# Kernel tuning notes

Measured on AMD Instinct MI355X. Metric: run time of the kernel, lower is better.

## Reference

```python
import jax, jax.numpy as jnp
import numpy as np

INPUT_SIZE = 1024
MEMORY_SIZE = 32768
MEMORY_DIM = 128
TOP_K = 32
EPS = 1e-8


def _linear_params(key, fan_in, fan_out):
    kw, kb = jax.random.split(key)
    bound = 1.0 / np.sqrt(fan_in)
    W = jax.random.uniform(kw, (fan_out, fan_in), jnp.float32, -bound, bound)
    b = jax.random.uniform(kb, (fan_out,), jnp.float32, -bound, bound)
    return W, b


def setup_inputs() -> dict:
    key = jax.random.key(0)
    kx, km, k1, k2, k3 = jax.random.split(key, 5)
    x = jax.random.normal(kx, (16, INPUT_SIZE), jnp.float32)
    # xavier_uniform for the memory table
    xav = np.sqrt(6.0 / (MEMORY_SIZE + MEMORY_DIM))
    memory = jax.random.uniform(km, (MEMORY_SIZE, MEMORY_DIM), jnp.float32, -xav, xav)
    Ww, bw = _linear_params(k1, INPUT_SIZE, MEMORY_DIM)   # write_proj
    Wr, br = _linear_params(k2, INPUT_SIZE, MEMORY_DIM)   # read_proj
    Wo, bo = _linear_params(k3, MEMORY_DIM, INPUT_SIZE)   # output_proj
    return {"x": x, "memory": memory, "Ww": Ww, "bw": bw,
            "Wr": Wr, "br": br, "Wo": Wo, "bo": bo}


def reference(x, memory, Ww, bw, Wr, br, Wo, bo):
    # x: [B, I]; memory: [M, D] (prev_memory=None path -> shared table per batch)
    write_vector = x @ Ww.T + bw          # [B, D]
    read_query = x @ Wr.T + br            # [B, D]

    # cosine similarity of each query against every memory slot: [B, M]
    qn = jnp.maximum(jnp.linalg.norm(read_query, axis=-1, keepdims=True), EPS)  # [B, 1]
    mn = jnp.maximum(jnp.linalg.norm(memory, axis=-1), EPS)                      # [M]
    similarity = (read_query @ memory.T) / (qn * mn[None, :])

    # top-k slots; the scatter-built one-hot bmm is just a gather + sum
    _, top_idx = jax.lax.top_k(similarity, TOP_K)        # [B, k] int32
    retrieved = memory[top_idx].sum(axis=1)              # [B, D]

    output = retrieved @ Wo.T + bo                        # [B, I]

    write_strength = jax.nn.sigmoid(
        jnp.sum(write_vector * retrieved, axis=-1, keepdims=True))  # [B, 1]
    # outer-product update [B,1,D] broadcast-added over all M slots
    update = (write_strength * write_vector)[:, None, :]  # [B, 1, D]
    new_memory = memory[None, :, :] + update              # [B, M, D]
    return output, new_memory
```

## Files before the change

### kernel.cpp

```cpp
#include <hip/hip_runtime.h>
#include <math.h>

#define BATCH 16
#define ISZ   1024
#define MSZ   32768
#define DSZ   128
#define TOPK  32
#define EPSV  1e-8f
#define NCHUNK 32
#define CHUNK  (MSZ / NCHUNK)
#define CPL    (CHUNK / 64)

__global__ void proj_kernel(const float* __restrict__ x,
                            const float* __restrict__ Ww, const float* __restrict__ bw,
                            const float* __restrict__ Wr, const float* __restrict__ br,
                            float* __restrict__ wv, float* __restrict__ rq) {
    int d = blockIdx.x;
    int b = blockIdx.y;
    int lane = threadIdx.x;
    const float* xr  = x  + (size_t)b * ISZ;
    const float* wwr = Ww + (size_t)d * ISZ;
    const float* wrr = Wr + (size_t)d * ISZ;
    float aw = 0.f, ar = 0.f;
    for (int j = lane; j < ISZ; j += 64) {
        float xv = xr[j];
        aw = fmaf(xv, wwr[j], aw);
        ar = fmaf(xv, wrr[j], ar);
    }
    for (int off = 32; off; off >>= 1) {
        aw += __shfl_down(aw, off);
        ar += __shfl_down(ar, off);
    }
    if (lane == 0) {
        wv[b * DSZ + d] = aw + bw[d];
        rq[b * DSZ + d] = ar + br[d];
    }
}

__global__ void mnorm_kernel(const float* __restrict__ memory, float* __restrict__ mn) {
    int wave = threadIdx.x >> 6;
    int lane = threadIdx.x & 63;
    int m = blockIdx.x * 4 + wave;
    const float* row = memory + (size_t)m * DSZ;
    float a = row[lane] * row[lane] + row[lane + 64] * row[lane + 64];
    for (int off = 32; off; off >>= 1) a += __shfl_down(a, off);
    if (lane == 0) mn[m] = fmaxf(sqrtf(a), EPSV);
}

__global__ __launch_bounds__(128)
void sim_kernel(const float* __restrict__ rq, const float* __restrict__ mn,
                const float* __restrict__ memory, float* __restrict__ sim) {
    __shared__ float qn_s[BATCH];
    int tid = threadIdx.x;
    {
        int b = tid >> 3, seg = tid & 7;
        float a = 0.f;
        #pragma unroll
        for (int j = 0; j < 16; ++j) {
            float v = rq[b * DSZ + seg * 16 + j];
            a = fmaf(v, v, a);
        }
        for (int off = 4; off; off >>= 1) a += __shfl_down(a, off, 8);
        if (seg == 0) qn_s[b] = fmaxf(sqrtf(a), EPSV);
    }
    __syncthreads();

    int r = blockIdx.x * 128 + tid;
    const float4* row = (const float4*)(memory + (size_t)r * DSZ);
    const float4* rq4 = (const float4*)rq;
    float acc[BATCH];
    #pragma unroll
    for (int b = 0; b < BATCH; ++b) acc[b] = 0.f;
    float mnr = mn[r];
    #pragma unroll 4
    for (int j = 0; j < 32; ++j) {
        float4 v = row[j];
        #pragma unroll
        for (int b = 0; b < BATCH; ++b) {
            float4 q = rq4[b * 32 + j];
            acc[b] = fmaf(v.x, q.x, fmaf(v.y, q.y, fmaf(v.z, q.z, fmaf(v.w, q.w, acc[b]))));
        }
    }
    #pragma unroll
    for (int b = 0; b < BATCH; ++b)
        sim[(size_t)b * MSZ + r] = acc[b] / (qn_s[b] * mnr);
}

__global__ __launch_bounds__(256)
void ptopk_kernel(const float* __restrict__ sim,
                  float* __restrict__ cand_v, int* __restrict__ cand_i) {
    int lane = threadIdx.x & 63;
    int task = blockIdx.x * 4 + (threadIdx.x >> 6);
    int b     = task >> 5;
    int chunk = task & 31;
    int base  = chunk * CHUNK;
    const float* s = sim + (size_t)b * MSZ + base;

    float val[CPL];
    #pragma unroll
    for (int i = 0; i < CPL; ++i) val[i] = s[i * 64 + lane];

    float lv = -INFINITY; int lm = -1;
    #pragma unroll
    for (int i = 0; i < CPL; ++i) if (val[i] > lv) { lv = val[i]; lm = i; }

    float keep_v = -INFINITY; int keep_i = 0x7FFFFFFF;
    for (int k = 0; k < TOPK; ++k) {
        float bv = lv;
        int   bi = (lm < 0) ? 0x7FFFFFFF : base + lm * 64 + lane;
        #pragma unroll
        for (int off = 32; off; off >>= 1) {
            float ov = __shfl_xor(bv, off);
            int   oi = __shfl_xor(bi, off);
            if (ov > bv || (ov == bv && oi < bi)) { bv = ov; bi = oi; }
        }
        if (lane == k) { keep_v = bv; keep_i = bi; }
        int rel = bi - base;
        if (rel >= 0 && (rel & 63) == lane && (rel >> 6) < CPL) {
            val[rel >> 6] = -INFINITY;
            lv = -INFINITY; lm = -1;
            #pragma unroll
            for (int i = 0; i < CPL; ++i) if (val[i] > lv) { lv = val[i]; lm = i; }
        }
    }
    if (lane < TOPK) {
        cand_v[task * TOPK + lane] = keep_v;
        cand_i[task * TOPK + lane] = keep_i;
    }
}

__global__ __launch_bounds__(128)
void merge_kernel(const float* __restrict__ cand_v, const int* __restrict__ cand_i,
                  const float* __restrict__ memory, const float* __restrict__ wv,
                  float* __restrict__ retrieved, float* __restrict__ u) {
    __shared__ int   topi[TOPK];
    __shared__ float r_s[DSZ];
    __shared__ float s_sh;
    int b = blockIdx.x;
    int tid = threadIdx.x;
    int lane = tid & 63;
    const int NC = NCHUNK * TOPK;
    const int PL = NC / 64;

    if (tid < 64) {
        float val[PL]; int idx[PL];
        #pragma unroll
        for (int i = 0; i < PL; ++i) {
            val[i] = cand_v[b * NC + i * 64 + lane];
            idx[i] = cand_i[b * NC + i * 64 + lane];
        }
        float lv; int li, lm;
        {
            lv = -INFINITY; li = 0x7FFFFFFF; lm = -1;
            #pragma unroll
            for (int i = 0; i < PL; ++i)
                if (val[i] > lv || (val[i] == lv && idx[i] < li)) { lv = val[i]; li = idx[i]; lm = i; }
        }
        float keep_v = -INFINITY; int keep_i = 0x7FFFFFFF;
        for (int k = 0; k < TOPK; ++k) {
            float bv = lv; int bi = li;
            #pragma unroll
            for (int off = 32; off; off >>= 1) {
                float ov = __shfl_xor(bv, off);
                int   oi = __shfl_xor(bi, off);
                if (ov > bv || (ov == bv && oi < bi)) { bv = ov; bi = oi; }
            }
            if (lane == k) { keep_v = bv; keep_i = bi; }
            if (bi == li && lm >= 0) {
                val[lm] = -INFINITY;
                lv = -INFINITY; li = 0x7FFFFFFF; lm = -1;
                #pragma unroll
                for (int i = 0; i < PL; ++i)
                    if (val[i] > lv || (val[i] == lv && idx[i] < li)) { lv = val[i]; li = idx[i]; lm = i; }
            }
        }
        if (lane < TOPK) topi[lane] = keep_i;
    }
    __syncthreads();

    float rsum = 0.f;
    for (int k = 0; k < TOPK; ++k)
        rsum += memory[(size_t)topi[k] * DSZ + tid];
    r_s[tid] = rsum;
    retrieved[b * DSZ + tid] = rsum;
    __syncthreads();

    if (tid < 64) {
        float a = wv[b * DSZ + tid] * r_s[tid] + wv[b * DSZ + 64 + tid] * r_s[64 + tid];
        for (int off = 32; off; off >>= 1) a += __shfl_down(a, off);
        if (tid == 0) s_sh = 1.f / (1.f + expf(-a));
    }
    __syncthreads();
    u[b * DSZ + tid] = s_sh * wv[b * DSZ + tid];
}

__global__ __launch_bounds__(128)
void out_kernel(const float* __restrict__ retrieved, const float* __restrict__ Wo,
                const float* __restrict__ bo, float* __restrict__ out) {
    __shared__ float r_s[DSZ];
    int b = blockIdx.y;
    int i = blockIdx.x * 128 + threadIdx.x;
    r_s[threadIdx.x] = retrieved[b * DSZ + threadIdx.x];
    __syncthreads();
    const float4* w4 = (const float4*)(Wo + (size_t)i * DSZ);
    const float4* r4 = (const float4*)r_s;
    float acc = 0.f;
    #pragma unroll 8
    for (int j = 0; j < 32; ++j) {
        float4 w = w4[j];
        float4 r = r4[j];
        acc = fmaf(w.x, r.x, fmaf(w.y, r.y, fmaf(w.z, r.z, fmaf(w.w, r.w, acc))));
    }
    out[b * ISZ + i] = acc + bo[i];
}

__global__ void bcast_kernel(const float* __restrict__ memory, const float* __restrict__ u,
                             float* __restrict__ out_nm) {
    __shared__ float4 u_s[BATCH * DSZ / 4];
    int tid = threadIdx.x;
    const float4* u4 = (const float4*)u;
    for (int i = tid; i < BATCH * DSZ / 4; i += 256) u_s[i] = u4[i];
    __syncthreads();
    size_t f = (size_t)blockIdx.x * 256 + tid;
    float4 m4 = ((const float4*)memory)[f];
    int d4 = (int)(f & 31);
    float4* o = (float4*)out_nm;
    #pragma unroll
    for (int b = 0; b < BATCH; ++b) {
        float4 uv = u_s[b * 32 + d4];
        float4 r = make_float4(m4.x + uv.x, m4.y + uv.y, m4.z + uv.z, m4.w + uv.w);
        o[(size_t)b * (MSZ * DSZ / 4) + f] = r;
    }
}

extern "C" void kernel_launch(void* const* d_in, const int* in_sizes, int n_in,
                              void* d_out, int out_size, void* d_ws, size_t ws_size,
                              hipStream_t stream) {
    const float* x      = (const float*)d_in[0];
    const float* memory = (const float*)d_in[1];
    const float* Ww     = (const float*)d_in[2];
    const float* bw     = (const float*)d_in[3];
    const float* Wr     = (const float*)d_in[4];
    const float* br     = (const float*)d_in[5];
    const float* Wo     = (const float*)d_in[6];
    const float* bo     = (const float*)d_in[7];

    float* out    = (float*)d_out;
    float* out_nm = out + BATCH * ISZ;

    float* ws        = (float*)d_ws;
    float* wv        = ws;
    float* rq        = wv + BATCH * DSZ;
    float* mn        = rq + BATCH * DSZ;
    float* sim       = mn + MSZ;
    float* cand_v    = sim + (size_t)BATCH * MSZ;
    int*   cand_i    = (int*)(cand_v + BATCH * NCHUNK * TOPK);
    float* retrieved = (float*)(cand_i + BATCH * NCHUNK * TOPK);
    float* u         = retrieved + BATCH * DSZ;

    proj_kernel<<<dim3(DSZ, BATCH), 64, 0, stream>>>(x, Ww, bw, Wr, br, wv, rq);
    mnorm_kernel<<<MSZ / 4, 256, 0, stream>>>(memory, mn);
    sim_kernel<<<MSZ / 128, 128, 0, stream>>>(rq, mn, memory, sim);
    ptopk_kernel<<<(BATCH * NCHUNK) / 4, 256, 0, stream>>>(sim, cand_v, cand_i);
    merge_kernel<<<BATCH, 128, 0, stream>>>(cand_v, cand_i, memory, wv, retrieved, u);
    out_kernel<<<dim3(8, BATCH), 128, 0, stream>>>(retrieved, Wo, bo, out);
    bcast_kernel<<<MSZ * DSZ / 4 / 256, 256, 0, stream>>>(memory, u, out_nm);
}
```

Baseline: 163.1 us.

## Fuse row-norm into similarity kernel and output projection into merge kernel

Row norms of the memory table are now accumulated inside the similarity kernel from the same loaded float4s, removing a separate pass over the memory table and one launch. The output projection is folded into the merge kernel, so each batch block computes all 1024 outputs from its retrieved vector in shared memory. This removes two launches and the intermediate buffers, but the output projection now runs on only 16 blocks, which reduces parallelism for the Wo read.

```diff
diff --git a/kernel.cpp b/kernel.cpp
--- a/kernel.cpp
+++ b/kernel.cpp
@@ -37,18 +37,8 @@
     }
 }
 
-__global__ void mnorm_kernel(const float* __restrict__ memory, float* __restrict__ mn) {
-    int wave = threadIdx.x >> 6;
-    int lane = threadIdx.x & 63;
-    int m = blockIdx.x * 4 + wave;
-    const float* row = memory + (size_t)m * DSZ;
-    float a = row[lane] * row[lane] + row[lane + 64] * row[lane + 64];
-    for (int off = 32; off; off >>= 1) a += __shfl_down(a, off);
-    if (lane == 0) mn[m] = fmaxf(sqrtf(a), EPSV);
-}
-
 __global__ __launch_bounds__(128)
-void sim_kernel(const float* __restrict__ rq, const float* __restrict__ mn,
+void sim_kernel(const float* __restrict__ rq,
                 const float* __restrict__ memory, float* __restrict__ sim) {
     __shared__ float qn_s[BATCH];
     int tid = threadIdx.x;
@@ -71,16 +61,18 @@
     float acc[BATCH];
     #pragma unroll
     for (int b = 0; b < BATCH; ++b) acc[b] = 0.f;
-    float mnr = mn[r];
+    float nrm = 0.f;
     #pragma unroll 4
     for (int j = 0; j < 32; ++j) {
         float4 v = row[j];
+        nrm = fmaf(v.x, v.x, fmaf(v.y, v.y, fmaf(v.z, v.z, fmaf(v.w, v.w, nrm))));
         #pragma unroll
         for (int b = 0; b < BATCH; ++b) {
             float4 q = rq4[b * 32 + j];
             acc[b] = fmaf(v.x, q.x, fmaf(v.y, q.y, fmaf(v.z, q.z, fmaf(v.w, q.w, acc[b]))));
         }
     }
+    float mnr = fmaxf(sqrtf(nrm), EPSV);
     #pragma unroll
     for (int b = 0; b < BATCH; ++b)
         sim[(size_t)b * MSZ + r] = acc[b] / (qn_s[b] * mnr);
@@ -132,7 +124,8 @@
 __global__ __launch_bounds__(128)
 void merge_kernel(const float* __restrict__ cand_v, const int* __restrict__ cand_i,
                   const float* __restrict__ memory, const float* __restrict__ wv,
-                  float* __restrict__ retrieved, float* __restrict__ u) {
+                  const float* __restrict__ Wo, const float* __restrict__ bo,
+                  float* __restrict__ out, float* __restrict__ u) {
     __shared__ int   topi[TOPK];
     __shared__ float r_s[DSZ];
     __shared__ float s_sh;
@@ -156,7 +149,7 @@
             for (int i = 0; i < PL; ++i)
                 if (val[i] > lv || (val[i] == lv && idx[i] < li)) { lv = val[i]; li = idx[i]; lm = i; }
         }
-        float keep_v = -INFINITY; int keep_i = 0x7FFFFFFF;
+        float keep_i_v = -INFINITY; int keep_i = 0x7FFFFFFF;
         for (int k = 0; k < TOPK; ++k) {
             float bv = lv; int bi = li;
             #pragma unroll
@@ -165,7 +158,7 @@
                 int   oi = __shfl_xor(bi, off);
                 if (ov > bv || (ov == bv && oi < bi)) { bv = ov; bi = oi; }
             }
-            if (lane == k) { keep_v = bv; keep_i = bi; }
+            if (lane == k) { keep_i_v = bv; keep_i = bi; }
             if (bi == li && lm >= 0) {
                 val[lm] = -INFINITY;
                 lv = -INFINITY; li = 0x7FFFFFFF; lm = -1;
@@ -174,6 +167,7 @@
                     if (val[i] > lv || (val[i] == lv && idx[i] < li)) { lv = val[i]; li = idx[i]; lm = i; }
             }
         }
+        (void)keep_i_v;
         if (lane < TOPK) topi[lane] = keep_i;
     }
     __syncthreads();
@@ -182,7 +176,6 @@
     for (int k = 0; k < TOPK; ++k)
         rsum += memory[(size_t)topi[k] * DSZ + tid];
     r_s[tid] = rsum;
-    retrieved[b * DSZ + tid] = rsum;
     __syncthreads();
 
     if (tid < 64) {
@@ -192,26 +185,21 @@
     }
     __syncthreads();
     u[b * DSZ + tid] = s_sh * wv[b * DSZ + tid];
-}
-
-__global__ __launch_bounds__(128)
-void out_kernel(const float* __restrict__ retrieved, const float* __restrict__ Wo,
-                const float* __restrict__ bo, float* __restrict__ out) {
-    __shared__ float r_s[DSZ];
-    int b = blockIdx.y;
-    int i = blockIdx.x * 128 + threadIdx.x;
-    r_s[threadIdx.x] = retrieved[b * DSZ + threadIdx.x];
-    __syncthreads();
-    const float4* w4 = (const float4*)(Wo + (size_t)i * DSZ);
+
     const float4* r4 = (const float4*)r_s;
-    float acc = 0.f;
-    #pragma unroll 8
-    for (int j = 0; j < 32; ++j) {
-        float4 w = w4[j];
-        float4 r = r4[j];
-        acc = fmaf(w.x, r.x, fmaf(w.y, r.y, fmaf(w.z, r.z, fmaf(w.w, r.w, acc))));
-    }
-    out[b * ISZ + i] = acc + bo[i];
+    float rloc[4];
+    for (int i = tid; i < ISZ; i += 128) {
+        const float4* w4 = (const float4*)(Wo + (size_t)i * DSZ);
+        float acc = 0.f;
+        #pragma unroll 8
+        for (int j = 0; j < 32; ++j) {
+            float4 w = w4[j];
+            float4 r = r4[j];
+            acc = fmaf(w.x, r.x, fmaf(w.y, r.y, fmaf(w.z, r.z, fmaf(w.w, r.w, acc))));
+        }
+        out[b * ISZ + i] = acc + bo[i];
+    }
+    (void)rloc;
 }
 
 __global__ void bcast_kernel(const float* __restrict__ memory, const float* __restrict__ u,
@@ -251,18 +239,14 @@
     float* ws        = (float*)d_ws;
     float* wv        = ws;
     float* rq        = wv + BATCH * DSZ;
-    float* mn        = rq + BATCH * DSZ;
-    float* sim       = mn + MSZ;
+    float* sim       = rq + BATCH * DSZ;
     float* cand_v    = sim + (size_t)BATCH * MSZ;
     int*   cand_i    = (int*)(cand_v + BATCH * NCHUNK * TOPK);
-    float* retrieved = (float*)(cand_i + BATCH * NCHUNK * TOPK);
-    float* u         = retrieved + BATCH * DSZ;
+    float* u         = (float*)(cand_i + BATCH * NCHUNK * TOPK);
 
     proj_kernel<<<dim3(DSZ, BATCH), 64, 0, stream>>>(x, Ww, bw, Wr, br, wv, rq);
-    mnorm_kernel<<<MSZ / 4, 256, 0, stream>>>(memory, mn);
-    sim_kernel<<<MSZ / 128, 128, 0, stream>>>(rq, mn, memory, sim);
+    sim_kernel<<<MSZ / 128, 128, 0, stream>>>(rq, memory, sim);
     ptopk_kernel<<<(BATCH * NCHUNK) / 4, 256, 0, stream>>>(sim, cand_v, cand_i);
-    merge_kernel<<<BATCH, 128, 0, stream>>>(cand_v, cand_i, memory, wv, retrieved, u);
-    out_kernel<<<dim3(8, BATCH), 128, 0, stream>>>(retrieved, Wo, bo, out);
+    merge_kernel<<<BATCH, 128, 0, stream>>>(cand_v, cand_i, memory, wv, Wo, bo, out, u);
     bcast_kernel<<<MSZ * DSZ / 4 / 256, 256, 0, stream>>>(memory, u, out_nm);
 }
```

Measured after the change: 167.0 us. +2.4%, slower.
